# Kernel tuning notes

Hardware: AMD Instinct MI355X
Metric: run time of the kernel (lower is better)

## Reference

```python
import jax, jax.numpy as jnp
import numpy as np
from jax.scipy.special import gammaln, xlogy

B, T, C = 1, 1536, 1536
H, K, V = 8, 64, 192   # heads, key size per head, value size per head (C // H)
F = 192                # num_relative_position_features (C // H)
LN_EPS = 1e-3          # keras LayerNormalization default


def _layer_norm(x, g, b):
    mu = jnp.mean(x, axis=-1, keepdims=True)
    var = jnp.var(x, axis=-1, keepdims=True)
    return (x - mu) * jax.lax.rsqrt(var + LN_EPS) * g + b


def _positional_features(positions, feature_size, seq_length):
    # 3 symmetric basis classes x 2 (symmetric + sign-asymmetric) = 6 components
    n = feature_size // 6
    ap = jnp.abs(positions)[:, None]  # [L, 1]
    # exponential half-life decay
    half_life = (2.0 ** np.linspace(3.0, np.log2(seq_length), n)).astype(np.float32)
    f_exp = jnp.exp(ap * (-(np.log(2.0) / half_life))[None, :].astype(np.float32))
    # central mask
    widths = (2.0 ** np.arange(1, n + 1) - 1.0).astype(np.float32)
    f_cm = (widths[None, :] > ap).astype(jnp.float32)
    # gamma pdf bumps
    stddev = seq_length / (2.0 * n)
    mean = np.linspace(seq_length / n, float(seq_length), n)
    conc = ((mean / stddev) ** 2).astype(np.float32)
    rate = (mean / stddev ** 2).astype(np.float32)
    log_unnorm = xlogy(conc - 1.0, ap) - rate * ap
    log_norm = (gammaln(conc) - conc * np.log(rate)).astype(np.float32)
    prob = jnp.exp(log_unnorm - log_norm) + 1e-8
    f_g = prob / jnp.max(prob, axis=1, keepdims=True)
    emb = jnp.concatenate([f_exp, f_cm, f_g], axis=-1)          # [L, F/2]
    emb = jnp.concatenate([emb, jnp.sign(positions)[:, None] * emb], axis=-1)
    return emb                                                   # [L, F]


def _relative_shift(x):
    # TransformerXL shift: [B,H,T,2T-1] -> [B,H,T,T]
    b, h, t1, t2 = x.shape
    x = jnp.pad(x, ((0, 0), (0, 0), (0, 0), (1, 0)))
    x = x.reshape(b, h, t2 + 1, t1)[:, :, 1:, :].reshape(b, h, t1, t2)
    return x[..., :(t2 + 1) // 2]


def _forward(x, ln1_g, ln1_b, ln2_g, ln2_b, Wq, Wk, Wv, Wr, Wo, bo,
             r_w_bias, r_r_bias, W1, b1, W2, b2):
    Bv, Tv, Cv = x.shape
    # --- multi-head attention with relative positions ---
    xn = _layer_norm(x, ln1_g, ln1_b)
    q = (xn @ Wq).reshape(Bv, Tv, H, K).transpose(0, 2, 1, 3) * (K ** -0.5)
    k = (xn @ Wk).reshape(Bv, Tv, H, K).transpose(0, 2, 1, 3)
    v = (xn @ Wv).reshape(Bv, Tv, H, V).transpose(0, 2, 1, 3)
    content = jnp.einsum('bhqk,bhmk->bhqm', q + r_w_bias, k)     # [B,H,T,T]
    distances = jnp.arange(-Tv + 1, Tv, dtype=jnp.float32)       # [2T-1]
    pos = _positional_features(distances, F, Tv)                 # [2T-1, F]
    r_k = (pos @ Wr).reshape(2 * Tv - 1, H, K).transpose(1, 0, 2)
    rel = jnp.einsum('bhqk,hmk->bhqm', q + r_r_bias, r_k)        # [B,H,T,2T-1]
    logits = content + _relative_shift(rel)
    attn = jax.nn.softmax(logits, axis=-1)
    o = jnp.einsum('bhqm,bhmv->bhqv', attn, v)
    o = o.transpose(0, 2, 1, 3).reshape(Bv, Tv, H * V) @ Wo + bo
    y = x + o
    # --- MLP ---
    yn = _layer_norm(y, ln2_g, ln2_b)
    h1 = jax.nn.relu(yn @ W1 + b1)
    return y + h1 @ W2 + b2


def setup_inputs() -> dict:
    key = jax.random.key(0)
    ks = jax.random.split(key, 10)
    nrm = lambda i, shape, s=0.02: jax.random.normal(ks[i], shape, jnp.float32) * s
    return {
        'x': jax.random.normal(ks[0], (B, T, C), jnp.float32),
        'ln1_g': jnp.ones((C,), jnp.float32), 'ln1_b': jnp.zeros((C,), jnp.float32),
        'ln2_g': jnp.ones((C,), jnp.float32), 'ln2_b': jnp.zeros((C,), jnp.float32),
        'Wq': nrm(1, (C, H * K)), 'Wk': nrm(2, (C, H * K)), 'Wv': nrm(3, (C, H * V)),
        'Wr': nrm(4, (F, H * K)), 'Wo': nrm(5, (H * V, C)),
        'bo': jnp.zeros((C,), jnp.float32),
        'r_w_bias': nrm(6, (1, H, 1, K), 0.1), 'r_r_bias': nrm(7, (1, H, 1, K), 0.1),
        'W1': nrm(8, (C, 2 * C)), 'b1': jnp.zeros((2 * C,), jnp.float32),
        'W2': nrm(9, (2 * C, C)), 'b2': jnp.zeros((C,), jnp.float32),
    }


def reference(x, ln1_g, ln1_b, ln2_g, ln2_b, Wq, Wk, Wv, Wr, Wo, bo,
              r_w_bias, r_r_bias, W1, b1, W2, b2):
    return _forward(x, ln1_g, ln1_b, ln2_g, ln2_b, Wq, Wk, Wv, Wr, Wo, bo,
                    r_w_bias, r_r_bias, W1, b1, W2, b2)
```

## Files before the change

### kernel.cpp

```cpp
#include <hip/hip_runtime.h>
#include <math.h>

#define TT 1536
#define CC 1536
#define NH 8
#define KD 64
#define VD 192
#define FD 192

typedef short bf16x8 __attribute__((ext_vector_type(8)));
typedef float f32x4 __attribute__((ext_vector_type(4)));

__device__ inline unsigned short f2bf(float x) {
    unsigned u = __float_as_uint(x);
    u += 0x7FFF + ((u >> 16) & 1);
    return (unsigned short)(u >> 16);
}
__device__ inline float bf2f(unsigned short b) {
    return __uint_as_float(((unsigned)b) << 16);
}
__device__ inline void gload16(const void* g, void* l) {
    __builtin_amdgcn_global_load_lds(
        (const __attribute__((address_space(1))) unsigned int*)g,
        (__attribute__((address_space(3))) unsigned int*)l, 16, 0, 0);
}
__device__ inline int swzo(int row, int chunk) { return (chunk ^ (row & 7)) << 3; }

template<int N> __device__ inline void vmwait() {
    if constexpr (N == 0)      asm volatile("s_waitcnt vmcnt(0)" ::: "memory");
    else if constexpr (N == 4) asm volatile("s_waitcnt vmcnt(4)" ::: "memory");
    else if constexpr (N == 6) asm volatile("s_waitcnt vmcnt(6)" ::: "memory");
    else                       asm volatile("s_waitcnt vmcnt(8)" ::: "memory");
}

__device__ inline void ln_row(const float* __restrict__ x,
                              const float* __restrict__ g,
                              const float* __restrict__ b,
                              unsigned short* __restrict__ out,
                              int row, int lane)
{
    const float* xr = x + (size_t)row * CC;
    unsigned short* orow = out + (size_t)row * CC;

    float4 V[6];
    float s = 0.f, ss = 0.f;
#pragma unroll
    for (int c = 0; c < 6; c++) {
        V[c] = *reinterpret_cast<const float4*>(&xr[c * 256 + lane * 4]);
        s  += V[c].x + V[c].y + V[c].z + V[c].w;
        ss += V[c].x * V[c].x + V[c].y * V[c].y + V[c].z * V[c].z + V[c].w * V[c].w;
    }
#pragma unroll
    for (int off = 32; off; off >>= 1) {
        s  += __shfl_xor(s, off);
        ss += __shfl_xor(ss, off);
    }
    float mean = s * (1.f / CC);
    float var  = ss * (1.f / CC) - mean * mean;
    float rstd = rsqrtf(fmaxf(var, 0.f) + 1e-3f);
#pragma unroll
    for (int c = 0; c < 6; c++) {
        float4 G = *reinterpret_cast<const float4*>(&g[c * 256 + lane * 4]);
        float4 B = *reinterpret_cast<const float4*>(&b[c * 256 + lane * 4]);
        ushort4 pk;
        pk.x = f2bf((V[c].x - mean) * rstd * G.x + B.x);
        pk.y = f2bf((V[c].y - mean) * rstd * G.y + B.y);
        pk.z = f2bf((V[c].z - mean) * rstd * G.z + B.z);
        pk.w = f2bf((V[c].w - mean) * rstd * G.w + B.w);
        *reinterpret_cast<ushort4*>(&orow[c * 256 + lane * 4]) = pk;
    }
}

__global__ __launch_bounds__(256)
void ln_kernel(const float* __restrict__ x, const float* __restrict__ g,
               const float* __restrict__ b, unsigned short* __restrict__ out)
{
    int wid = threadIdx.x >> 6, lane = threadIdx.x & 63;
    ln_row(x, g, b, out, blockIdx.x * 4 + wid, lane);
}

struct WCD { const float* W; unsigned short* Wt; int Kw, Nw, t0; };
struct WCP { WCD e[7]; };
#define WCONV_BLKS 15456
#define LN1_BLKS   384
#define POS_BLKS   (2 * TT - 1)

__global__ __launch_bounds__(256)
void prep_all(WCP p, const float* __restrict__ x,
              const float* __restrict__ ln1_g, const float* __restrict__ ln1_b,
              unsigned short* __restrict__ xnb, unsigned short* __restrict__ pos)
{
    int bid = blockIdx.x;
    int tid = threadIdx.x;

    if (bid < WCONV_BLKS) {
        __shared__ float t[32][33];
        int i = 0;
#pragma unroll
        for (int j = 1; j < 7; j++) if (bid >= p.e[j].t0) i = j;
        const float* W = p.e[i].W;
        unsigned short* Wt = p.e[i].Wt;
        int Kw = p.e[i].Kw, Nw = p.e[i].Nw;
        int local = bid - p.e[i].t0;
        int tpx = Nw >> 5;
        int n0 = (local % tpx) * 32, k0 = (local / tpx) * 32;

        int r = tid >> 3, c4 = (tid & 7) * 4;
        float4 v = *reinterpret_cast<const float4*>(&W[(size_t)(k0 + r) * Nw + n0 + c4]);
        t[r][c4 + 0] = v.x; t[r][c4 + 1] = v.y; t[r][c4 + 2] = v.z; t[r][c4 + 3] = v.w;
        __syncthreads();
        ushort4 pk;
        pk.x = f2bf(t[c4 + 0][r]);
        pk.y = f2bf(t[c4 + 1][r]);
        pk.z = f2bf(t[c4 + 2][r]);
        pk.w = f2bf(t[c4 + 3][r]);
        *reinterpret_cast<ushort4*>(&Wt[(size_t)(n0 + r) * Kw + k0 + c4]) = pk;
        return;
    }

    if (bid < WCONV_BLKS + LN1_BLKS) {
        int grp = bid - WCONV_BLKS;
        int wid = tid >> 6, lane = tid & 63;
        ln_row(x, ln1_g, ln1_b, xnb, grp * 4 + wid, lane);
        return;
    }

    {
        int l = bid - (WCONV_BLKS + LN1_BLKS);
        float pp = (float)(l - (TT - 1));
        float ap = fabsf(pp);
        float sgn = (pp > 0.f) ? 1.f : ((pp < 0.f) ? -1.f : 0.f);

        __shared__ float gp[32];
        __shared__ float gmax_s;
        if (tid < 32) {
            int j = tid;
            double conc = 4.0 * (double)(j + 1) * (double)(j + 1);
            double rate = (double)(j + 1) / 12.0;
            double log_norm = lgamma(conc) - conc * log(rate);
            double prob;
            if (ap == 0.f) prob = 1e-8;
            else prob = exp((conc - 1.0) * log((double)ap) - rate * (double)ap - log_norm) + 1e-8;
            gp[j] = (float)prob;
        }
        __syncthreads();
        if (tid == 0) {
            float m = gp[0];
            for (int j = 1; j < 32; j++) m = fmaxf(m, gp[j]);
            gmax_s = m;
        }
        __syncthreads();
        if (tid < 96) {
            int cls = tid / 32, j = tid % 32;
            float val;
            if (cls == 0) {
                double step = (10.584962500721156 - 3.0) / 31.0;
                double hl = exp2(3.0 + j * step);
                val = (float)exp(-(double)ap * 0.6931471805599453 / hl);
            } else if (cls == 1) {
                float width = exp2f((float)(j + 1)) - 1.f;
                val = (width > ap) ? 1.f : 0.f;
            } else {
                val = gp[j] / gmax_s;
            }
            pos[(size_t)l * FD + tid] = f2bf(val);
            pos[(size_t)l * FD + 96 + tid] = f2bf(sgn * val);
        }
    }
}

template<int TM, int TN>
__global__ __launch_bounds__(256)
void gemm_bf16(const unsigned short* __restrict__ A,
               const unsigned short* __restrict__ Bt,
               void* __restrict__ Cv, unsigned short* __restrict__ C2,
               unsigned short* __restrict__ C3,
               int M, int N, int K, int lda, int ldb, int ldc,
               long sA, long sB, long sC,
               float alpha, const float* __restrict__ bias,
               const float* __restrict__ bias2,
               const float* __restrict__ resid,
               int mode, int relu, int head_ndiv, int xm)
{
    constexpr int WM = TM / 2, WN = TN / 2;
    constexpr int MF = WM / 16, NF = WN / 16;
    constexpr int LPT = TM / 32 + TN / 32;
    __shared__ unsigned short lA[2][TM * 64];
    __shared__ unsigned short lB[2][TN * 64];

    int tid = threadIdx.x;
    int w = tid >> 6, l = tid & 63;

    int gx = gridDim.x, gy = gridDim.y;
    int d = blockIdx.y * gx + blockIdx.x;
    int bx, by;
    if (xm) {
        int xn = 8 / xm;
        int cm = gy / xm, cn = gx / xn;
        int xcd = d & 7, local = d >> 3;
        int bxl = local / cm, byl = local % cm;
        by = (xcd / xn) * cm + byl;
        bx = (xcd % xn) * cn + bxl;
    } else {
        int nwg = gx * gy;
        int work = d;
        if ((nwg & 7) == 0) work = (d & 7) * (nwg >> 3) + (d >> 3);
        bx = work % gx;
        by = work / gx;
    }

    int n0 = bx * TN;
    int m0 = by * TM;
    if (head_ndiv) {
        A += (size_t)(n0 / head_ndiv) * sA;
    } else {
        A  += (size_t)blockIdx.z * sA;
        Bt += (size_t)blockIdx.z * sB;
    }
    int R0 = (w & 1) * WM, C0 = (w >> 1) * WN;
    int lrow = l >> 3;
    int lsw = ((l & 7) ^ lrow) << 3;
    int l15 = l & 15, lg = l >> 4;

    f32x4 acc[MF][NF] = {};

    const int NSTEP = K >> 6;

    auto STAGE = [&](int t, int buf) {
        int k0 = t << 6;
#pragma unroll
        for (int q = 0; q < TM / 32; q++) {
            int r0 = w * (TM / 4) + q * 8;
            gload16(A + (size_t)(m0 + r0 + lrow) * lda + k0 + lsw, &lA[buf][r0 * 64]);
        }
#pragma unroll
        for (int q = 0; q < TN / 32; q++) {
            int r0 = w * (TN / 4) + q * 8;
            gload16(Bt + (size_t)(n0 + r0 + lrow) * ldb + k0 + lsw, &lB[buf][r0 * 64]);
        }
    };

    STAGE(0, 0);

    int cur = 0;
    for (int t = 0; t < NSTEP; ++t) {
        if (t + 1 < NSTEP) {
            STAGE(t + 1, cur ^ 1);
            vmwait<LPT>();
        } else {
            vmwait<0>();
        }
        __builtin_amdgcn_s_barrier();
        __builtin_amdgcn_sched_barrier(0);

#pragma unroll
        for (int kk = 0; kk < 2; kk++) {
            int ch = kk * 4 + lg;
            bf16x8 av[MF], bv[NF];
#pragma unroll
            for (int m = 0; m < MF; m++) {
                int row = R0 + m * 16 + l15;
                av[m] = *(const bf16x8*)&lA[cur][row * 64 + swzo(row, ch)];
            }
#pragma unroll
            for (int n = 0; n < NF; n++) {
                int row = C0 + n * 16 + l15;
                bv[n] = *(const bf16x8*)&lB[cur][row * 64 + swzo(row, ch)];
            }
#pragma unroll
            for (int m = 0; m < MF; m++)
#pragma unroll
                for (int n = 0; n < NF; n++)
                    acc[m][n] = __builtin_amdgcn_mfma_f32_16x16x32_bf16(av[m], bv[n], acc[m][n], 0, 0, 0);
        }
        __builtin_amdgcn_s_barrier();
        cur ^= 1;
    }

    int rb = m0 + R0 + lg * 4;
    int cb = n0 + C0 + l15;

    if (mode == 4) {
        unsigned short* qw = (unsigned short*)Cv;
#pragma unroll
        for (int m = 0; m < MF; m++) {
            int rowb = rb + m * 16;
#pragma unroll
            for (int n = 0; n < NF; n++) {
                int col = cb + n * 16;
                if (col < 512) {
#pragma unroll
                    for (int reg = 0; reg < 4; reg++) {
                        int row = rowb + reg;
                        float v = alpha * acc[m][n][reg];
                        qw[(size_t)row * 512 + col] = f2bf(v + bias[col]);
                        C2[(size_t)row * 512 + col] = f2bf(v + bias2[col]);
                    }
                } else if (col < 1024) {
                    unsigned short* kb = C3;
#pragma unroll
                    for (int reg = 0; reg < 4; reg++)
                        kb[(size_t)(rowb + reg) * 512 + col - 512] = f2bf(acc[m][n][reg]);
                } else {
                    unsigned short* vT = (unsigned short*)(void*)(C3 + (size_t)1536 * 512);
                    int vc = col - 1024;
                    ushort4 pk;
                    pk.x = f2bf(acc[m][n][0]);
                    pk.y = f2bf(acc[m][n][1]);
                    pk.z = f2bf(acc[m][n][2]);
                    pk.w = f2bf(acc[m][n][3]);
                    *reinterpret_cast<ushort4*>(&vT[(size_t)vc * 1536 + rowb]) = pk;
                }
            }
        }
        return;
    }

#pragma unroll
    for (int m = 0; m < MF; m++) {
#pragma unroll
        for (int n = 0; n < NF; n++) {
            int col = cb + n * 16;
            if (col >= N) continue;
            float bs = bias ? bias[col] : 0.f;
#pragma unroll
            for (int reg = 0; reg < 4; reg++) {
                int row = rb + m * 16 + reg;
                if (row >= M) continue;
                float v = alpha * acc[m][n][reg] + bs;
                if (resid) v += resid[(size_t)row * ldc + col];
                if (relu)  v = fmaxf(v, 0.f);
                if (mode == 1) {
                    unsigned short* C = (unsigned short*)Cv + (size_t)blockIdx.z * sC;
                    C[(size_t)row * ldc + col] = f2bf(v);
                } else {
                    float* C = (float*)Cv + (size_t)blockIdx.z * sC;
                    C[(size_t)row * ldc + col] = v;
                }
            }
        }
    }
}

__global__ __launch_bounds__(256)
void logits_mfma(const unsigned short* __restrict__ qw,
                 const unsigned short* __restrict__ qr,
                 const unsigned short* __restrict__ kmat,
                 const unsigned short* __restrict__ rk,
                 unsigned short* __restrict__ out)
{
    __shared__ unsigned short pool[3 * 64 * 64 + 128 * 64];
    unsigned short* lQw = pool;
    unsigned short* lQr = pool + 64 * 64;
    unsigned short* lK  = pool + 2 * 64 * 64;
    unsigned short* lR  = pool + 3 * 64 * 64;
    unsigned short* lC2 = pool;

    int j0 = blockIdx.x * 64;
    int i0 = blockIdx.y * 64;
    int h  = blockIdx.z;
    int tid = threadIdx.x;
    int w = tid >> 6, l = tid & 63;
    int lrow = l >> 3;
    int lsw = ((l & 7) ^ lrow) << 3;
    int l15 = l & 15, lg = l >> 4;
    int obase = j0 - i0 + 1472;

#pragma unroll
    for (int q = 0; q < 2; q++) {
        int r0 = w * 16 + q * 8;
        gload16(qw   + (size_t)(i0 + r0 + lrow) * (NH * KD) + h * KD + lsw, &lQw[r0 * 64]);
        gload16(qr   + (size_t)(i0 + r0 + lrow) * (NH * KD) + h * KD + lsw, &lQr[r0 * 64]);
        gload16(kmat + (size_t)(j0 + r0 + lrow) * (NH * KD) + h * KD + lsw, &lK [r0 * 64]);
    }
#pragma unroll
    for (int q = 0; q < 4; q++) {
        int r0 = w * 32 + q * 8;
        gload16(rk + (size_t)(obase + r0 + lrow) * (NH * KD) + h * KD + lsw, &lR[r0 * 64]);
    }
    __syncthreads();

    f32x4 acc1[4] = {};
    f32x4 acc2[8] = {};
#pragma unroll
    for (int kk = 0; kk < 2; kk++) {
        int ch = kk * 4 + lg;
        int qrow = 16 * w + l15;
        bf16x8 av  = *(const bf16x8*)&lQw[qrow * 64 + swzo(qrow, ch)];
        bf16x8 arv = *(const bf16x8*)&lQr[qrow * 64 + swzo(qrow, ch)];
#pragma unroll
        for (int n = 0; n < 4; n++) {
            int row = n * 16 + l15;
            bf16x8 bv = *(const bf16x8*)&lK[row * 64 + swzo(row, ch)];
            acc1[n] = __builtin_amdgcn_mfma_f32_16x16x32_bf16(av, bv, acc1[n], 0, 0, 0);
        }
#pragma unroll
        for (int n = 0; n < 8; n++) {
            int row = n * 16 + l15;
            bf16x8 rv = *(const bf16x8*)&lR[row * 64 + swzo(row, ch)];
            acc2[n] = __builtin_amdgcn_mfma_f32_16x16x32_bf16(arv, rv, acc2[n], 0, 0, 0);
        }
    }
    __syncthreads();

#pragma unroll
    for (int n = 0; n < 8; n++)
#pragma unroll
        for (int reg = 0; reg < 4; reg++)
            lC2[(16 * w + lg * 4 + reg) * 128 + n * 16 + l15] = f2bf(acc2[n][reg]);
    __syncthreads();

#pragma unroll
    for (int n = 0; n < 4; n++) {
#pragma unroll
        for (int reg = 0; reg < 4; reg++) {
            int u = 16 * w + lg * 4 + reg;
            int v = n * 16 + l15;
            float val = acc1[n][reg] + bf2f(lC2[u * 128 + 63 + v - u]);
            out[((size_t)h * TT + i0 + u) * TT + j0 + v] = f2bf(val);
        }
    }
}

__global__ __launch_bounds__(256)
void softmax_bf16(unsigned short* __restrict__ P)
{
    int wid = threadIdx.x >> 6, lane = threadIdx.x & 63;
    size_t r = (size_t)blockIdx.x * 4 + wid;
    unsigned* row = (unsigned*)(P + r * TT);

    uint4 U[3];
    float v[24];
    float m = -1e30f;
#pragma unroll
    for (int c = 0; c < 3; c++) {
        U[c] = *reinterpret_cast<const uint4*>(&row[c * 256 + lane * 4]);
        const unsigned* pd = (const unsigned*)&U[c];
#pragma unroll
        for (int d = 0; d < 4; d++) {
            float lo = bf2f((unsigned short)(pd[d] & 0xFFFF));
            float hi = bf2f((unsigned short)(pd[d] >> 16));
            v[c * 8 + 2 * d]     = lo;
            v[c * 8 + 2 * d + 1] = hi;
            m = fmaxf(m, fmaxf(lo, hi));
        }
    }
#pragma unroll
    for (int off = 32; off; off >>= 1) m = fmaxf(m, __shfl_xor(m, off));
    float s = 0.f;
#pragma unroll
    for (int i = 0; i < 24; i++) { v[i] = __expf(v[i] - m); s += v[i]; }
#pragma unroll
    for (int off = 32; off; off >>= 1) s += __shfl_xor(s, off);
    float inv = 1.f / s;
#pragma unroll
    for (int c = 0; c < 3; c++) {
        unsigned* pd = (unsigned*)&U[c];
#pragma unroll
        for (int d = 0; d < 4; d++)
            pd[d] = (unsigned)f2bf(v[c * 8 + 2 * d] * inv)
                  | ((unsigned)f2bf(v[c * 8 + 2 * d + 1] * inv) << 16);
        *reinterpret_cast<uint4*>(&row[c * 256 + lane * 4]) = U[c];
    }
}

extern "C" void kernel_launch(void* const* d_in, const int* in_sizes, int n_in,
                              void* d_out, int out_size, void* d_ws, size_t ws_size,
                              hipStream_t stream)
{
    const float* x     = (const float*)d_in[0];
    const float* ln1_g = (const float*)d_in[1];
    const float* ln1_b = (const float*)d_in[2];
    const float* ln2_g = (const float*)d_in[3];
    const float* ln2_b = (const float*)d_in[4];
    const float* Wq    = (const float*)d_in[5];
    const float* Wk    = (const float*)d_in[6];
    const float* Wv    = (const float*)d_in[7];
    const float* Wr    = (const float*)d_in[8];
    const float* Wo    = (const float*)d_in[9];
    const float* bo    = (const float*)d_in[10];
    const float* rwb   = (const float*)d_in[11];
    const float* rrb   = (const float*)d_in[12];
    const float* W1    = (const float*)d_in[13];
    const float* b1    = (const float*)d_in[14];
    const float* W2    = (const float*)d_in[15];
    const float* b2    = (const float*)d_in[16];
    float* out = (float*)d_out;

    char* w8 = (char*)d_ws;
    unsigned short* xnb  = (unsigned short*)(w8 + 0);
    unsigned short* qwb  = (unsigned short*)(w8 + 4718592);
    unsigned short* qrb  = (unsigned short*)(w8 + 6291456);
    unsigned short* kbb  = (unsigned short*)(w8 + 7864320);
    unsigned short* vTb  = (unsigned short*)(w8 + 9437184);
    unsigned short* posb = (unsigned short*)(w8 + 14155776);
    unsigned short* rkb  = (unsigned short*)(w8 + 15335424);
    unsigned short* Pb   = (unsigned short*)(w8 + 18481152);
    unsigned short* ob   = (unsigned short*)(w8 + 56229888);
    float*          yb   = (float*)        (w8 + 60948480);
    unsigned short* WqkvT= (unsigned short*)(w8 + 70385664);
    unsigned short* WrT  = (unsigned short*)(w8 + 78249984);
    unsigned short* WoT  = (unsigned short*)(w8 + 78446592);
    unsigned short* W1T  = (unsigned short*)(w8 + 83165184);
    unsigned short* W2T  = (unsigned short*)(w8 + 92602368);
    unsigned short* h1b  = Pb;
    unsigned short* ynb  = xnb;

    WCP wp;
    wp.e[0] = { Wq, WqkvT,                       1536, 512,      0 };
    wp.e[1] = { Wk, WqkvT + (size_t)512 * 1536,  1536, 512,    768 };
    wp.e[2] = { Wv, WqkvT + (size_t)1024 * 1536, 1536, 1536,  1536 };
    wp.e[3] = { Wr, WrT,                          192, 512,   3840 };
    wp.e[4] = { Wo, WoT,                         1536, 1536,  3936 };
    wp.e[5] = { W1, W1T,                         1536, 3072,  6240 };
    wp.e[6] = { W2, W2T,                         3072, 1536, 10848 };
    prep_all<<<WCONV_BLKS + LN1_BLKS + POS_BLKS, 256, 0, stream>>>(
        wp, x, ln1_g, ln1_b, xnb, posb);

    gemm_bf16<64, 128><<<dim3(20, 24, 1), 256, 0, stream>>>(xnb, WqkvT, qwb, qrb, kbb,
        1536, 2560, 1536, 1536, 1536, 0, 0, 0, 0,
        0.125f, rwb, rrb, nullptr, 4, 0, 0, 2);

    gemm_bf16<64, 128><<<dim3(4, 48, 1), 256, 0, stream>>>(posb, WrT, rkb, nullptr, nullptr,
        3071, 512, 192, 192, 192, 512, 0, 0, 0,
        1.f, nullptr, nullptr, nullptr, 1, 0, 0, 2);

    logits_mfma<<<dim3(24, 24, 8), 256, 0, stream>>>(qwb, qrb, kbb, rkb, Pb);
    softmax_bf16<<<NH * TT / 4, 256, 0, stream>>>(Pb);

    gemm_bf16<64, 64><<<dim3(24, 24, 1), 256, 0, stream>>>(Pb, vTb, ob, nullptr, nullptr,
        1536, 1536, 1536, 1536, 1536, 1536, (long)TT * TT, 0, 0,
        1.f, nullptr, nullptr, nullptr, 1, 0, VD, 2);

    gemm_bf16<64, 64><<<dim3(24, 24, 1), 256, 0, stream>>>(ob, WoT, yb, nullptr, nullptr,
        1536, 1536, 1536, 1536, 1536, 1536, 0, 0, 0,
        1.f, bo, nullptr, x, 0, 0, 0, 2);

    ln_kernel<<<TT / 4, 256, 0, stream>>>(yb, ln2_g, ln2_b, ynb);

    gemm_bf16<64, 128><<<dim3(24, 24, 1), 256, 0, stream>>>(ynb, W1T, h1b, nullptr, nullptr,
        1536, 3072, 1536, 1536, 1536, 3072, 0, 0, 0,
        1.f, b1, nullptr, nullptr, 1, 1, 0, 2);

    gemm_bf16<64, 64><<<dim3(24, 24, 1), 256, 0, stream>>>(h1b, W2T, out, nullptr, nullptr,
        1536, 1536, 3072, 3072, 3072, 1536, 0, 0, 0,
        1.f, b2, nullptr, yb, 0, 0, 0, 4);
}
```

Before: 209.7 us.

## Fuse relative-position logits, softmax and PV into one flash-attention kernel

Replaces the separate logits kernel, in-place softmax pass and batched P·V GEMM with a single flash-style kernel. Each block handles 32 query rows of one head and streams 64-key tiles of K, relative keys and V with an online softmax. The relative shift is done through LDS. This removes the round trip of the 8×1536×1536 bf16 logits matrix to memory and two launches. In exchange it uses only 384 blocks with several barriers per tile and cross-wave reductions through LDS, so occupancy and latency hiding may suffer.

```diff
diff --git a/kernel.cpp b/kernel.cpp
--- a/kernel.cpp
+++ b/kernel.cpp
@@ -31,6 +31,9 @@
     else if constexpr (N == 4) asm volatile("s_waitcnt vmcnt(4)" ::: "memory");
     else if constexpr (N == 6) asm volatile("s_waitcnt vmcnt(6)" ::: "memory");
     else                       asm volatile("s_waitcnt vmcnt(8)" ::: "memory");
+}
+__device__ inline void lgkmwait0() {
+    asm volatile("s_waitcnt lgkmcnt(0)" ::: "memory");
 }
 
 __device__ inline void ln_row(const float* __restrict__ x,
@@ -342,126 +345,242 @@
     }
 }
 
+#define AOF_QW 0
+#define AOF_QR 2048
+#define AOF_P  0
+#define AOF_RED 2048
+#define AOF_K  4096
+#define AOF_RK 8192
+#define AOF_V  16384
+#define AOF_R  28672
+
 __global__ __launch_bounds__(256)
-void logits_mfma(const unsigned short* __restrict__ qw,
-                 const unsigned short* __restrict__ qr,
-                 const unsigned short* __restrict__ kmat,
-                 const unsigned short* __restrict__ rk,
-                 unsigned short* __restrict__ out)
+void attn_flash(const unsigned short* __restrict__ qw,
+                const unsigned short* __restrict__ qr,
+                const unsigned short* __restrict__ kmat,
+                const unsigned short* __restrict__ rkb,
+                const unsigned short* __restrict__ vT,
+                unsigned short* __restrict__ ob)
 {
-    __shared__ unsigned short pool[3 * 64 * 64 + 128 * 64];
-    unsigned short* lQw = pool;
-    unsigned short* lQr = pool + 64 * 64;
-    unsigned short* lK  = pool + 2 * 64 * 64;
-    unsigned short* lR  = pool + 3 * 64 * 64;
-    unsigned short* lC2 = pool;
-
-    int j0 = blockIdx.x * 64;
-    int i0 = blockIdx.y * 64;
-    int h  = blockIdx.z;
+    __shared__ unsigned short pool[32768];
+    int i0 = blockIdx.x * 32;
+    int h  = blockIdx.y;
     int tid = threadIdx.x;
     int w = tid >> 6, l = tid & 63;
     int lrow = l >> 3;
     int lsw = ((l & 7) ^ lrow) << 3;
     int l15 = l & 15, lg = l >> 4;
-    int obase = j0 - i0 + 1472;
-
-#pragma unroll
-    for (int q = 0; q < 2; q++) {
-        int r0 = w * 16 + q * 8;
-        gload16(qw   + (size_t)(i0 + r0 + lrow) * (NH * KD) + h * KD + lsw, &lQw[r0 * 64]);
-        gload16(qr   + (size_t)(i0 + r0 + lrow) * (NH * KD) + h * KD + lsw, &lQr[r0 * 64]);
-        gload16(kmat + (size_t)(j0 + r0 + lrow) * (NH * KD) + h * KD + lsw, &lK [r0 * 64]);
-    }
-#pragma unroll
-    for (int q = 0; q < 4; q++) {
-        int r0 = w * 32 + q * 8;
-        gload16(rk + (size_t)(obase + r0 + lrow) * (NH * KD) + h * KD + lsw, &lR[r0 * 64]);
-    }
-    __syncthreads();
-
-    f32x4 acc1[4] = {};
-    f32x4 acc2[8] = {};
-#pragma unroll
-    for (int kk = 0; kk < 2; kk++) {
-        int ch = kk * 4 + lg;
-        int qrow = 16 * w + l15;
-        bf16x8 av  = *(const bf16x8*)&lQw[qrow * 64 + swzo(qrow, ch)];
-        bf16x8 arv = *(const bf16x8*)&lQr[qrow * 64 + swzo(qrow, ch)];
-#pragma unroll
-        for (int n = 0; n < 4; n++) {
-            int row = n * 16 + l15;
-            bf16x8 bv = *(const bf16x8*)&lK[row * 64 + swzo(row, ch)];
-            acc1[n] = __builtin_amdgcn_mfma_f32_16x16x32_bf16(av, bv, acc1[n], 0, 0, 0);
-        }
-#pragma unroll
-        for (int n = 0; n < 8; n++) {
-            int row = n * 16 + l15;
-            bf16x8 rv = *(const bf16x8*)&lR[row * 64 + swzo(row, ch)];
-            acc2[n] = __builtin_amdgcn_mfma_f32_16x16x32_bf16(arv, rv, acc2[n], 0, 0, 0);
-        }
-    }
-    __syncthreads();
-
-#pragma unroll
-    for (int n = 0; n < 8; n++)
-#pragma unroll
-        for (int reg = 0; reg < 4; reg++)
-            lC2[(16 * w + lg * 4 + reg) * 128 + n * 16 + l15] = f2bf(acc2[n][reg]);
-    __syncthreads();
-
-#pragma unroll
-    for (int n = 0; n < 4; n++) {
-#pragma unroll
-        for (int reg = 0; reg < 4; reg++) {
-            int u = 16 * w + lg * 4 + reg;
-            int v = n * 16 + l15;
-            float val = acc1[n][reg] + bf2f(lC2[u * 128 + 63 + v - u]);
-            out[((size_t)h * TT + i0 + u) * TT + j0 + v] = f2bf(val);
-        }
-    }
-}
-
-__global__ __launch_bounds__(256)
-void softmax_bf16(unsigned short* __restrict__ P)
-{
-    int wid = threadIdx.x >> 6, lane = threadIdx.x & 63;
-    size_t r = (size_t)blockIdx.x * 4 + wid;
-    unsigned* row = (unsigned*)(P + r * TT);
-
-    uint4 U[3];
-    float v[24];
-    float m = -1e30f;
-#pragma unroll
-    for (int c = 0; c < 3; c++) {
-        U[c] = *reinterpret_cast<const uint4*>(&row[c * 256 + lane * 4]);
-        const unsigned* pd = (const unsigned*)&U[c];
-#pragma unroll
-        for (int d = 0; d < 4; d++) {
-            float lo = bf2f((unsigned short)(pd[d] & 0xFFFF));
-            float hi = bf2f((unsigned short)(pd[d] >> 16));
-            v[c * 8 + 2 * d]     = lo;
-            v[c * 8 + 2 * d + 1] = hi;
-            m = fmaxf(m, fmaxf(lo, hi));
-        }
-    }
-#pragma unroll
-    for (int off = 32; off; off >>= 1) m = fmaxf(m, __shfl_xor(m, off));
-    float s = 0.f;
-#pragma unroll
-    for (int i = 0; i < 24; i++) { v[i] = __expf(v[i] - m); s += v[i]; }
-#pragma unroll
-    for (int off = 32; off; off >>= 1) s += __shfl_xor(s, off);
-    float inv = 1.f / s;
-#pragma unroll
-    for (int c = 0; c < 3; c++) {
-        unsigned* pd = (unsigned*)&U[c];
-#pragma unroll
-        for (int d = 0; d < 4; d++)
-            pd[d] = (unsigned)f2bf(v[c * 8 + 2 * d] * inv)
-                  | ((unsigned)f2bf(v[c * 8 + 2 * d + 1] * inv) << 16);
-        *reinterpret_cast<uint4*>(&row[c * 256 + lane * 4]) = U[c];
-    }
+
+    auto stageK = [&](int j0) {
+#pragma unroll
+        for (int q = 0; q < 2; q++) {
+            int r0 = w * 16 + q * 8;
+            gload16(kmat + (size_t)(j0 + r0 + lrow) * 512 + h * KD + lsw, &pool[AOF_K + r0 * 64]);
+        }
+    };
+    auto stageRK = [&](int j0) {
+        int ob32 = j0 - i0 + 1504;
+#pragma unroll
+        for (int q = 0; q < 4; q++) {
+            int r0 = w * 32 + q * 8;
+            gload16(rkb + (size_t)(ob32 + r0 + lrow) * 512 + h * KD + lsw, &pool[AOF_RK + r0 * 64]);
+        }
+    };
+    auto stageV = [&](int j0) {
+#pragma unroll
+        for (int q = 0; q < 6; q++) {
+            int r0 = w * 48 + q * 8;
+            gload16(vT + (size_t)(h * VD + r0 + lrow) * 1536 + j0 + lsw, &pool[AOF_V + r0 * 64]);
+        }
+    };
+
+    gload16(qw + (size_t)(i0 + w * 8 + lrow) * 512 + h * KD + lsw, &pool[AOF_QW + (w * 8) * 64]);
+    gload16(qr + (size_t)(i0 + w * 8 + lrow) * 512 + h * KD + lsw, &pool[AOF_QR + (w * 8) * 64]);
+    stageK(0); stageRK(0);
+    vmwait<0>();
+    __builtin_amdgcn_s_barrier();
+    __builtin_amdgcn_sched_barrier(0);
+
+    bf16x8 qwf[2][2], qrf[2][2];
+#pragma unroll
+    for (int m = 0; m < 2; m++)
+#pragma unroll
+        for (int kk = 0; kk < 2; kk++) {
+            int row = m * 16 + l15;
+            qwf[m][kk] = *(const bf16x8*)&pool[AOF_QW + row * 64 + swzo(row, kk * 4 + lg)];
+            qrf[m][kk] = *(const bf16x8*)&pool[AOF_QR + row * 64 + swzo(row, kk * 4 + lg)];
+        }
+    lgkmwait0();
+
+    f32x4 accO[2][3] = {};
+    float m_run[2][4], l_run[2][4];
+#pragma unroll
+    for (int m = 0; m < 2; m++)
+#pragma unroll
+        for (int r = 0; r < 4; r++) { m_run[m][r] = -3e38f; l_run[m][r] = 0.f; }
+
+    float* redm = (float*)&pool[AOF_RED];
+    float* reds = redm + 128;
+    unsigned short* Rl = &pool[AOF_R];
+    unsigned short* Pl = &pool[AOF_P];
+    int v = w * 16 + l15;
+
+    for (int jt = 0; jt < 24; ++jt) {
+        int j0 = jt * 64;
+        vmwait<0>();
+        __builtin_amdgcn_s_barrier();
+        __builtin_amdgcn_sched_barrier(0);
+        stageV(j0);
+
+        f32x4 acc1[2] = {};
+        f32x4 acc2[2][2] = {};
+#pragma unroll
+        for (int kk = 0; kk < 2; kk++) {
+            int ch = kk * 4 + lg;
+            int krow = w * 16 + l15;
+            bf16x8 kv = *(const bf16x8*)&pool[AOF_K + krow * 64 + swzo(krow, ch)];
+#pragma unroll
+            for (int m = 0; m < 2; m++)
+                acc1[m] = __builtin_amdgcn_mfma_f32_16x16x32_bf16(qwf[m][kk], kv, acc1[m], 0, 0, 0);
+#pragma unroll
+            for (int n = 0; n < 2; n++) {
+                int rrow = w * 32 + n * 16 + l15;
+                bf16x8 rv = *(const bf16x8*)&pool[AOF_RK + rrow * 64 + swzo(rrow, ch)];
+#pragma unroll
+                for (int m = 0; m < 2; m++)
+                    acc2[m][n] = __builtin_amdgcn_mfma_f32_16x16x32_bf16(qrf[m][kk], rv, acc2[m][n], 0, 0, 0);
+            }
+        }
+#pragma unroll
+        for (int m = 0; m < 2; m++)
+#pragma unroll
+            for (int n = 0; n < 2; n++)
+#pragma unroll
+                for (int r = 0; r < 4; r++) {
+                    int u = m * 16 + lg * 4 + r;
+                    int c = w * 32 + n * 16 + l15;
+                    int off = (((c >> 3) ^ (u & 7)) << 3) + (c & 7);
+                    Rl[u * 128 + off] = f2bf(acc2[m][n][r]);
+                }
+        lgkmwait0();
+        __builtin_amdgcn_s_barrier();
+        __builtin_amdgcn_sched_barrier(0);
+        if (jt < 23) { stageK(j0 + 64); stageRK(j0 + 64); }
+
+        float s[2][4], pmax[2][4];
+#pragma unroll
+        for (int m = 0; m < 2; m++)
+#pragma unroll
+            for (int r = 0; r < 4; r++) {
+                int u = m * 16 + lg * 4 + r;
+                int c = 31 + v - u;
+                int off = (((c >> 3) ^ (u & 7)) << 3) + (c & 7);
+                s[m][r] = acc1[m][r] + bf2f(Rl[u * 128 + off]);
+                pmax[m][r] = s[m][r];
+            }
+#pragma unroll
+        for (int off = 8; off; off >>= 1)
+#pragma unroll
+            for (int m = 0; m < 2; m++)
+#pragma unroll
+                for (int r = 0; r < 4; r++)
+                    pmax[m][r] = fmaxf(pmax[m][r], __shfl_xor(pmax[m][r], off));
+        if (l15 == 0) {
+#pragma unroll
+            for (int m = 0; m < 2; m++)
+#pragma unroll
+                for (int r = 0; r < 4; r++)
+                    redm[(m * 16 + lg * 4 + r) * 4 + w] = pmax[m][r];
+        }
+        lgkmwait0();
+        __builtin_amdgcn_s_barrier();
+        __builtin_amdgcn_sched_barrier(0);
+
+        float scale[2][4], psum[2][4];
+#pragma unroll
+        for (int m = 0; m < 2; m++)
+#pragma unroll
+            for (int r = 0; r < 4; r++) {
+                int u = m * 16 + lg * 4 + r;
+                f32x4 mm = *(f32x4*)&redm[u * 4];
+                float mt = fmaxf(fmaxf(mm[0], mm[1]), fmaxf(mm[2], mm[3]));
+                float mn = fmaxf(m_run[m][r], mt);
+                scale[m][r] = __expf(m_run[m][r] - mn);
+                m_run[m][r] = mn;
+                float p = __expf(s[m][r] - mn);
+                psum[m][r] = p;
+                int off = (((v >> 3) ^ (u & 7)) << 3) + (v & 7);
+                Pl[u * 64 + off] = f2bf(p);
+            }
+#pragma unroll
+        for (int m = 0; m < 2; m++) {
+#pragma unroll
+            for (int n = 0; n < 3; n++)
+#pragma unroll
+                for (int r = 0; r < 4; r++)
+                    accO[m][n][r] *= scale[m][r];
+#pragma unroll
+            for (int r = 0; r < 4; r++) l_run[m][r] *= scale[m][r];
+        }
+#pragma unroll
+        for (int off = 8; off; off >>= 1)
+#pragma unroll
+            for (int m = 0; m < 2; m++)
+#pragma unroll
+                for (int r = 0; r < 4; r++)
+                    psum[m][r] += __shfl_xor(psum[m][r], off);
+        if (l15 == 0) {
+#pragma unroll
+            for (int m = 0; m < 2; m++)
+#pragma unroll
+                for (int r = 0; r < 4; r++)
+                    reds[(m * 16 + lg * 4 + r) * 4 + w] = psum[m][r];
+        }
+        if (jt < 23) vmwait<6>(); else vmwait<0>();
+        lgkmwait0();
+        __builtin_amdgcn_s_barrier();
+        __builtin_amdgcn_sched_barrier(0);
+
+#pragma unroll
+        for (int m = 0; m < 2; m++)
+#pragma unroll
+            for (int r = 0; r < 4; r++) {
+                int u = m * 16 + lg * 4 + r;
+                f32x4 sm = *(f32x4*)&reds[u * 4];
+                l_run[m][r] += sm[0] + sm[1] + sm[2] + sm[3];
+            }
+#pragma unroll
+        for (int kk = 0; kk < 2; kk++) {
+            int ch = kk * 4 + lg;
+            bf16x8 pa[2];
+#pragma unroll
+            for (int m = 0; m < 2; m++) {
+                int row = m * 16 + l15;
+                pa[m] = *(const bf16x8*)&Pl[row * 64 + swzo(row, ch)];
+            }
+#pragma unroll
+            for (int n = 0; n < 3; n++) {
+                int vrow = w * 48 + n * 16 + l15;
+                bf16x8 vv = *(const bf16x8*)&pool[AOF_V + vrow * 64 + swzo(vrow, ch)];
+#pragma unroll
+                for (int m = 0; m < 2; m++)
+                    accO[m][n] = __builtin_amdgcn_mfma_f32_16x16x32_bf16(pa[m], vv, accO[m][n], 0, 0, 0);
+            }
+        }
+    }
+
+#pragma unroll
+    for (int m = 0; m < 2; m++)
+#pragma unroll
+        for (int r = 0; r < 4; r++) {
+            int row = i0 + m * 16 + lg * 4 + r;
+            float inv = 1.f / l_run[m][r];
+#pragma unroll
+            for (int n = 0; n < 3; n++) {
+                int col = h * VD + w * 48 + n * 16 + l15;
+                ob[(size_t)row * 1536 + col] = f2bf(accO[m][n][r] * inv);
+            }
+        }
 }
 
 extern "C" void kernel_launch(void* const* d_in, const int* in_sizes, int n_in,
@@ -525,12 +644,7 @@
         3071, 512, 192, 192, 192, 512, 0, 0, 0,
         1.f, nullptr, nullptr, nullptr, 1, 0, 0, 2);
 
-    logits_mfma<<<dim3(24, 24, 8), 256, 0, stream>>>(qwb, qrb, kbb, rkb, Pb);
-    softmax_bf16<<<NH * TT / 4, 256, 0, stream>>>(Pb);
-
-    gemm_bf16<64, 64><<<dim3(24, 24, 1), 256, 0, stream>>>(Pb, vTb, ob, nullptr, nullptr,
-        1536, 1536, 1536, 1536, 1536, 1536, (long)TT * TT, 0, 0,
-        1.f, nullptr, nullptr, nullptr, 1, 0, VD, 2);
+    attn_flash<<<dim3(48, 8), 256, 0, stream>>>(qwb, qrb, kbb, rkb, vTb, ob);
 
     gemm_bf16<64, 64><<<dim3(24, 24, 1), 256, 0, stream>>>(ob, WoT, yb, nullptr, nullptr,
         1536, 1536, 1536, 1536, 1536, 1536, 0, 0, 0,
```

Result: slower. 257.4 us (+22.8%).

## Fuse QKV and positional GEMMs into one launch; split-K final FFN GEMM with atomics

Applied to the files above, without the earlier changes.

The QKV projection GEMM and the relative-position key GEMM now run as one dual-problem launch through a shared device-level GEMM core, which removes a kernel launch and lets the small positional GEMM fill CUs left idle by the larger one. The second FFN GEMM is split along K into two halves (grid z=2), and each half accumulates into the output with float atomicAdd. The LN2 kernel pre-initialises the output with residual plus bias b2 so the atomics can add onto it. The split doubles parallelism for a K=3072 GEMM with only 576 tiles, at the cost of atomic traffic and a summation order that is no longer deterministic.

```diff
diff --git a/kernel.cpp b/kernel.cpp
--- a/kernel.cpp
+++ b/kernel.cpp
@@ -37,7 +37,9 @@
                               const float* __restrict__ g,
                               const float* __restrict__ b,
                               unsigned short* __restrict__ out,
-                              int row, int lane)
+                              int row, int lane,
+                              const float* __restrict__ add_b,
+                              float* __restrict__ oinit)
 {
     const float* xr = x + (size_t)row * CC;
     unsigned short* orow = out + (size_t)row * CC;
@@ -68,15 +70,23 @@
         pk.z = f2bf((V[c].z - mean) * rstd * G.z + B.z);
         pk.w = f2bf((V[c].w - mean) * rstd * G.w + B.w);
         *reinterpret_cast<ushort4*>(&orow[c * 256 + lane * 4]) = pk;
+        if (oinit) {
+            float4 A2 = *reinterpret_cast<const float4*>(&add_b[c * 256 + lane * 4]);
+            float4 o;
+            o.x = V[c].x + A2.x; o.y = V[c].y + A2.y;
+            o.z = V[c].z + A2.z; o.w = V[c].w + A2.w;
+            *reinterpret_cast<float4*>(&oinit[(size_t)row * CC + c * 256 + lane * 4]) = o;
+        }
     }
 }
 
 __global__ __launch_bounds__(256)
 void ln_kernel(const float* __restrict__ x, const float* __restrict__ g,
-               const float* __restrict__ b, unsigned short* __restrict__ out)
+               const float* __restrict__ b, unsigned short* __restrict__ out,
+               const float* __restrict__ add_b, float* __restrict__ oinit)
 {
     int wid = threadIdx.x >> 6, lane = threadIdx.x & 63;
-    ln_row(x, g, b, out, blockIdx.x * 4 + wid, lane);
+    ln_row(x, g, b, out, blockIdx.x * 4 + wid, lane, add_b, oinit);
 }
 
 struct WCD { const float* W; unsigned short* Wt; int Kw, Nw, t0; };
@@ -121,7 +131,7 @@
     if (bid < WCONV_BLKS + LN1_BLKS) {
         int grp = bid - WCONV_BLKS;
         int wid = tid >> 6, lane = tid & 63;
-        ln_row(x, ln1_g, ln1_b, xnb, grp * 4 + wid, lane);
+        ln_row(x, ln1_g, ln1_b, xnb, grp * 4 + wid, lane, nullptr, nullptr);
         return;
     }
 
@@ -170,17 +180,17 @@
 }
 
 template<int TM, int TN>
-__global__ __launch_bounds__(256)
-void gemm_bf16(const unsigned short* __restrict__ A,
-               const unsigned short* __restrict__ Bt,
-               void* __restrict__ Cv, unsigned short* __restrict__ C2,
-               unsigned short* __restrict__ C3,
-               int M, int N, int K, int lda, int ldb, int ldc,
-               long sA, long sB, long sC,
-               float alpha, const float* __restrict__ bias,
-               const float* __restrict__ bias2,
-               const float* __restrict__ resid,
-               int mode, int relu, int head_ndiv, int xm)
+__device__ void gemm_core(const unsigned short* __restrict__ A,
+                          const unsigned short* __restrict__ Bt,
+                          void* __restrict__ Cv, unsigned short* __restrict__ C2,
+                          unsigned short* __restrict__ C3,
+                          int M, int N, int K, int lda, int ldb, int ldc,
+                          long sA, long sB, long sC,
+                          float alpha, const float* __restrict__ bias,
+                          const float* __restrict__ bias2,
+                          const float* __restrict__ resid,
+                          int mode, int relu, int head_ndiv, int xm,
+                          int gx, int gy, int d, int bz)
 {
     constexpr int WM = TM / 2, WN = TN / 2;
     constexpr int MF = WM / 16, NF = WN / 16;
@@ -191,8 +201,6 @@
     int tid = threadIdx.x;
     int w = tid >> 6, l = tid & 63;
 
-    int gx = gridDim.x, gy = gridDim.y;
-    int d = blockIdx.y * gx + blockIdx.x;
     int bx, by;
     if (xm) {
         int xn = 8 / xm;
@@ -214,8 +222,8 @@
     if (head_ndiv) {
         A += (size_t)(n0 / head_ndiv) * sA;
     } else {
-        A  += (size_t)blockIdx.z * sA;
-        Bt += (size_t)blockIdx.z * sB;
+        A  += (size_t)bz * sA;
+        Bt += (size_t)bz * sB;
     }
     int R0 = (w & 1) * WM, C0 = (w >> 1) * WN;
     int lrow = l >> 3;
@@ -316,6 +324,23 @@
         return;
     }
 
+    if (mode == 5) {
+        float* C = (float*)Cv;
+#pragma unroll
+        for (int m = 0; m < MF; m++) {
+#pragma unroll
+            for (int n = 0; n < NF; n++) {
+                int col = cb + n * 16;
+#pragma unroll
+                for (int reg = 0; reg < 4; reg++) {
+                    int row = rb + m * 16 + reg;
+                    atomicAdd(&C[(size_t)row * ldc + col], alpha * acc[m][n][reg]);
+                }
+            }
+        }
+        return;
+    }
+
 #pragma unroll
     for (int m = 0; m < MF; m++) {
 #pragma unroll
@@ -331,14 +356,60 @@
                 if (resid) v += resid[(size_t)row * ldc + col];
                 if (relu)  v = fmaxf(v, 0.f);
                 if (mode == 1) {
-                    unsigned short* C = (unsigned short*)Cv + (size_t)blockIdx.z * sC;
+                    unsigned short* C = (unsigned short*)Cv + (size_t)bz * sC;
                     C[(size_t)row * ldc + col] = f2bf(v);
                 } else {
-                    float* C = (float*)Cv + (size_t)blockIdx.z * sC;
+                    float* C = (float*)Cv + (size_t)bz * sC;
                     C[(size_t)row * ldc + col] = v;
                 }
             }
         }
+    }
+}
+
+template<int TM, int TN>
+__global__ __launch_bounds__(256)
+void gemm_bf16(const unsigned short* __restrict__ A,
+               const unsigned short* __restrict__ Bt,
+               void* __restrict__ Cv, unsigned short* __restrict__ C2,
+               unsigned short* __restrict__ C3,
+               int M, int N, int K, int lda, int ldb, int ldc,
+               long sA, long sB, long sC,
+               float alpha, const float* __restrict__ bias,
+               const float* __restrict__ bias2,
+               const float* __restrict__ resid,
+               int mode, int relu, int head_ndiv, int xm)
+{
+    int d = blockIdx.y * gridDim.x + blockIdx.x;
+    gemm_core<TM, TN>(A, Bt, Cv, C2, C3, M, N, K, lda, ldb, ldc, sA, sB, sC,
+                      alpha, bias, bias2, resid, mode, relu, head_ndiv, xm,
+                      gridDim.x, gridDim.y, d, blockIdx.z);
+}
+
+struct GP {
+    const unsigned short *A, *Bt;
+    void* Cv; unsigned short *C2, *C3;
+    int M, N, K, lda, ldb, ldc;
+    long sA, sB, sC;
+    float alpha;
+    const float *bias, *bias2, *resid;
+    int mode, relu, head_ndiv, xm, gx, gy;
+};
+
+__global__ __launch_bounds__(256)
+void gemm_dual128(GP a, GP b, int nblk0)
+{
+    int bid = blockIdx.x;
+    if (bid < nblk0) {
+        gemm_core<64, 128>(a.A, a.Bt, a.Cv, a.C2, a.C3, a.M, a.N, a.K,
+                           a.lda, a.ldb, a.ldc, a.sA, a.sB, a.sC, a.alpha,
+                           a.bias, a.bias2, a.resid, a.mode, a.relu,
+                           a.head_ndiv, a.xm, a.gx, a.gy, bid, 0);
+    } else {
+        gemm_core<64, 128>(b.A, b.Bt, b.Cv, b.C2, b.C3, b.M, b.N, b.K,
+                           b.lda, b.ldb, b.ldc, b.sA, b.sB, b.sC, b.alpha,
+                           b.bias, b.bias2, b.resid, b.mode, b.relu,
+                           b.head_ndiv, b.xm, b.gx, b.gy, bid - nblk0, 0);
     }
 }
 
@@ -517,13 +588,17 @@
     prep_all<<<WCONV_BLKS + LN1_BLKS + POS_BLKS, 256, 0, stream>>>(
         wp, x, ln1_g, ln1_b, xnb, posb);
 
-    gemm_bf16<64, 128><<<dim3(20, 24, 1), 256, 0, stream>>>(xnb, WqkvT, qwb, qrb, kbb,
-        1536, 2560, 1536, 1536, 1536, 0, 0, 0, 0,
-        0.125f, rwb, rrb, nullptr, 4, 0, 0, 2);
-
-    gemm_bf16<64, 128><<<dim3(4, 48, 1), 256, 0, stream>>>(posb, WrT, rkb, nullptr, nullptr,
-        3071, 512, 192, 192, 192, 512, 0, 0, 0,
-        1.f, nullptr, nullptr, nullptr, 1, 0, 0, 2);
+    GP ga = { xnb, WqkvT, qwb, qrb, kbb,
+              1536, 2560, 1536, 1536, 1536, 0,
+              0, 0, 0,
+              0.125f, rwb, rrb, nullptr,
+              4, 0, 0, 2, 20, 24 };
+    GP gb = { posb, WrT, rkb, nullptr, nullptr,
+              3071, 512, 192, 192, 192, 512,
+              0, 0, 0,
+              1.f, nullptr, nullptr, nullptr,
+              1, 0, 0, 2, 4, 48 };
+    gemm_dual128<<<672, 256, 0, stream>>>(ga, gb, 480);
 
     logits_mfma<<<dim3(24, 24, 8), 256, 0, stream>>>(qwb, qrb, kbb, rkb, Pb);
     softmax_bf16<<<NH * TT / 4, 256, 0, stream>>>(Pb);
@@ -536,13 +611,13 @@
         1536, 1536, 1536, 1536, 1536, 1536, 0, 0, 0,
         1.f, bo, nullptr, x, 0, 0, 0, 2);
 
-    ln_kernel<<<TT / 4, 256, 0, stream>>>(yb, ln2_g, ln2_b, ynb);
+    ln_kernel<<<TT / 4, 256, 0, stream>>>(yb, ln2_g, ln2_b, ynb, b2, out);
 
     gemm_bf16<64, 128><<<dim3(24, 24, 1), 256, 0, stream>>>(ynb, W1T, h1b, nullptr, nullptr,
         1536, 3072, 1536, 1536, 1536, 3072, 0, 0, 0,
         1.f, b1, nullptr, nullptr, 1, 1, 0, 2);
 
-    gemm_bf16<64, 64><<<dim3(24, 24, 1), 256, 0, stream>>>(h1b, W2T, out, nullptr, nullptr,
-        1536, 1536, 3072, 3072, 3072, 1536, 0, 0, 0,
-        1.f, b2, nullptr, yb, 0, 0, 0, 4);
-}
+    gemm_bf16<64, 64><<<dim3(24, 24, 2), 256, 0, stream>>>(h1b, W2T, out, nullptr, nullptr,
+        1536, 1536, 1536, 3072, 3072, 1536, 1536, 1536, 0,
+        1.f, nullptr, nullptr, nullptr, 5, 0, 0, 4);
+}
```

Measured after the change: 209.3 us. No clear change (-0.2%).
